# Performance work log

Hardware: AMD Instinct MI355X
Metric: run time of the kernel (lower is better)

Reference implementation:

```python
import jax, jax.numpy as jnp
import numpy as np

# SymBranch: delta_i = |h_i - h_pi(i)| (0 if unpaired) -> ResNetMLP -> per-graph
# mean pairwise-L2 scores -> softmax(s/tau) -> weighted sum pooling.
# ResNetMLP (reconstructed, eval mode: dropout=identity):
#   h = x @ W_in + b_in
#   for each block: h = h + relu(LN(h @ Wk + bk))
#   z = LN_out(h @ W_out + b_out)   (last_norm=True)

B, NPG, IN_DIM, HID, EMB, NBLK = 64, 1024, 64, 256, 128, 3
TAU = 0.25
LN_EPS = 1e-5


def _ln(x, g, b):
    mu = jnp.mean(x, axis=-1, keepdims=True)
    var = jnp.var(x, axis=-1, keepdims=True)
    return (x - mu) * jax.lax.rsqrt(var + LN_EPS) * g + b


def setup_inputs() -> dict:
    key = jax.random.key(0)
    ks = jax.random.split(key, 8)
    N = B * NPG
    H = jax.random.normal(ks[0], (N, IN_DIM), jnp.float32)
    batch_ptr = jnp.arange(B + 1, dtype=jnp.int32) * NPG  # equal-size graphs
    # symmetric pairs: node i in first half of each graph paired with i + NPG/2
    half = NPG // 2
    base = (jnp.arange(B, dtype=jnp.int32) * NPG)[:, None]
    li = (base + jnp.arange(half, dtype=jnp.int32)[None, :]).reshape(-1)
    ri = (base + half + jnp.arange(half, dtype=jnp.int32)[None, :]).reshape(-1)
    pairs = jnp.stack([li, ri], axis=1)  # [M,2] global indices
    W_in = jax.random.normal(ks[1], (IN_DIM, HID), jnp.float32) * (1.0 / np.sqrt(IN_DIM))
    b_in = jnp.zeros((HID,), jnp.float32)
    Wb = jax.random.normal(ks[2], (NBLK, HID, HID), jnp.float32) * (1.0 / np.sqrt(HID))
    bb = jnp.zeros((NBLK, HID), jnp.float32)
    lng = jnp.ones((NBLK, HID), jnp.float32)
    lnb = jnp.zeros((NBLK, HID), jnp.float32)
    W_out = jax.random.normal(ks[3], (HID, EMB), jnp.float32) * (1.0 / np.sqrt(HID))
    b_out = jnp.zeros((EMB,), jnp.float32)
    lnf_g = jnp.ones((EMB,), jnp.float32)
    lnf_b = jnp.zeros((EMB,), jnp.float32)
    return dict(H=H, batch_ptr=batch_ptr, pairs=pairs, W_in=W_in, b_in=b_in,
                Wb=Wb, bb=bb, lng=lng, lnb=lnb, W_out=W_out, b_out=b_out,
                lnf_g=lnf_g, lnf_b=lnf_b)


def reference(H, batch_ptr, pairs, W_in, b_in, Wb, bb, lng, lnb, W_out, b_out, lnf_g, lnf_b):
    # gather-diff-scatter: delta_i = |h_i - h_pair(i)|, 0 for unpaired nodes
    li, ri = pairs[:, 0], pairs[:, 1]
    diff = jnp.abs(H[li] - H[ri])                       # [M, in_dim]
    delta = jnp.zeros_like(H).at[li].set(diff).at[ri].set(diff)  # [N, in_dim]
    # ResNetMLP (eval: dropout off)
    h = delta @ W_in + b_in                             # [N, HID]
    for k in range(NBLK):
        h = h + jax.nn.relu(_ln(h @ Wb[k] + bb[k], lng[k], lnb[k]))
    z = _ln(h @ W_out + b_out, lnf_g, lnf_b)            # [N, EMB]
    # per-graph mean pairwise L2 (graphs are equal-sized: reshape is the batched
    # equivalent of the python loop over batch_ptr slices)
    zb = z.reshape(B, NPG, EMB)
    sq = jnp.sum(zb * zb, axis=-1)                      # [B, n]
    d2 = sq[:, :, None] + sq[:, None, :] - 2.0 * jnp.einsum('bne,bme->bnm', zb, zb)
    dist = jnp.sqrt(jnp.clip(d2, 1e-12))                # [B, n, n]
    s = jnp.mean(dist, axis=-1)                         # [B, n]
    w = jax.nn.softmax(s / TAU, axis=-1)                # [B, n]
    f = jnp.einsum('bn,bne->be', w, zb)                 # [B, EMB]
    return f, w
```

## Files before the change

### kernel.cpp

```cpp
#include <hip/hip_runtime.h>
#include <hip/hip_bf16.h>

using bf16 = __hip_bfloat16;
typedef __attribute__((ext_vector_type(8))) short  bfrag;
typedef __attribute__((ext_vector_type(4))) float  ffrag;

#define DEVFN static __device__ __forceinline__

constexpr int BATCH  = 64;
constexpr int NPG    = 1024;
constexpr int IN_DIM = 64;
constexpr int HID    = 256;
constexpr int EMB    = 128;
constexpr int NPAIR  = BATCH * NPG / 2;
constexpr float TAU    = 0.25f;
constexpr float LN_EPS = 1e-5f;

constexpr int LDH = 264;

DEVFN float b2f(unsigned short u) {
    union { unsigned int i; float f; } x; x.i = ((unsigned int)u) << 16; return x.f;
}
DEVFN unsigned short f2b(float f) {
    bf16 h = __float2bfloat16(f);
    unsigned short u; __builtin_memcpy(&u, &h, 2); return u;
}

__global__ __launch_bounds__(256) void prep_w_kernel(
    const float* __restrict__ Win, const float* __restrict__ Wb,
    const float* __restrict__ Wout,
    unsigned short* __restrict__ WinT, unsigned short* __restrict__ WbT,
    unsigned short* __restrict__ WoutT)
{
    __shared__ short t[64][72];
    const int bid = blockIdx.x, tid = threadIdx.x;
    const float* S; unsigned short* D; int N_, K_, k0, n0;
    if (bid < 48) {
        int mat = bid >> 4, tt = bid & 15;
        S = Wb + mat * 65536; D = WbT + mat * 65536;
        K_ = 256; N_ = 256; k0 = (tt >> 2) * 64; n0 = (tt & 3) * 64;
    } else if (bid < 52) {
        int tt = bid - 48;
        S = Win; D = WinT; K_ = 64; N_ = 256; k0 = 0; n0 = tt * 64;
    } else {
        int tt = bid - 52;
        S = Wout; D = WoutT; K_ = 256; N_ = 128; k0 = (tt >> 1) * 64; n0 = (tt & 1) * 64;
    }
    #pragma unroll
    for (int it = 0; it < 4; ++it) {
        int idx = it * 256 + tid;
        int kk = idx >> 4, n4 = idx & 15;
        float4 v = *(const float4*)(S + (size_t)(k0 + kk) * N_ + n0 + n4 * 4);
        t[n4 * 4 + 0][kk] = (short)f2b(v.x);
        t[n4 * 4 + 1][kk] = (short)f2b(v.y);
        t[n4 * 4 + 2][kk] = (short)f2b(v.z);
        t[n4 * 4 + 3][kk] = (short)f2b(v.w);
    }
    __syncthreads();
    const int KB = K_ >> 5, nb = n0 >> 6;
    #pragma unroll
    for (int it = 0; it < 2; ++it) {
        int u = it * 256 + tid;
        int kbL = u >> 8, rem = u & 255;
        int j = rem >> 6, ln = rem & 63;
        int l16 = ln & 15, qd = ln >> 4;
        bfrag val = *(const bfrag*)&t[j * 16 + l16][kbL * 32 + qd * 8];
        size_t dst = (((size_t)(nb * KB + (k0 >> 5) + kbL) * 4 + j) * 64 + ln) * 8;
        *(bfrag*)(D + dst) = val;
    }
}

template<int K, int N, int MODE>
DEVFN void gemm_phase(short* hbuf, float (*part)[8],
                      const unsigned short* __restrict__ Bf,
                      const float* __restrict__ bias,
                      const float* __restrict__ gamma,
                      const float* __restrict__ beta,
                      unsigned short* __restrict__ Zb,
                      float* __restrict__ sqout, int m0)
{
    constexpr int WN = N / 64;
    constexpr int WM = 4 / WN;
    constexpr int RM = (64 / WM) / 16;
    constexpr int RN = 4;
    constexpr int KB = K / 32;

    const int tid  = threadIdx.x;
    const int wave = tid >> 6, lane = tid & 63;
    const int quad = lane >> 4, l16 = lane & 15;
    const int wrow = (wave / WN) * (64 / WM);
    const int wcol = (wave % WN) * 64;

    __syncthreads();

    ffrag acc[RM][RN];
    #pragma unroll
    for (int i = 0; i < RM; i++)
        #pragma unroll
        for (int j = 0; j < RN; j++)
            #pragma unroll
            for (int r = 0; r < 4; r++) acc[i][j][r] = 0.f;

    const unsigned short* bq = Bf + (size_t)(wcol >> 6) * KB * 2048
                                  + (size_t)lane * 8;

    bfrag acur[RM], bcur[RN];
    #pragma unroll
    for (int j = 0; j < RN; j++)
        bcur[j] = *(const bfrag*)(bq + j * 512);
    #pragma unroll
    for (int i = 0; i < RM; i++)
        acur[i] = *(const bfrag*)&hbuf[(wrow + i * 16 + l16) * LDH + quad * 8];

    #pragma unroll
    for (int kb = 0; kb < KB; kb++) {
        bfrag anx[RM], bnx[RN];
        if (kb + 1 < KB) {
            #pragma unroll
            for (int j = 0; j < RN; j++)
                bnx[j] = *(const bfrag*)(bq + ((kb + 1) * 4 + j) * 512);
            #pragma unroll
            for (int i = 0; i < RM; i++)
                anx[i] = *(const bfrag*)&hbuf[(wrow + i * 16 + l16) * LDH
                                              + (kb + 1) * 32 + quad * 8];
        }
        #pragma unroll
        for (int i = 0; i < RM; i++)
            #pragma unroll
            for (int j = 0; j < RN; j++)
                acc[i][j] = __builtin_amdgcn_mfma_f32_16x16x32_bf16(
                                acur[i], bcur[j], acc[i][j], 0, 0, 0);
        if (kb + 1 < KB) {
            #pragma unroll
            for (int i = 0; i < RM; i++) acur[i] = anx[i];
            #pragma unroll
            for (int j = 0; j < RN; j++) bcur[j] = bnx[j];
        }
    }

    float bia[RN], gam[RN], bet[RN];
    #pragma unroll
    for (int j = 0; j < RN; j++) {
        int gcol = wcol + j * 16 + l16;
        bia[j] = bias[gcol];
        if constexpr (MODE != 0) { gam[j] = gamma[gcol]; bet[j] = beta[gcol]; }
    }
    #pragma unroll
    for (int i = 0; i < RM; i++)
        #pragma unroll
        for (int j = 0; j < RN; j++)
            #pragma unroll
            for (int r = 0; r < 4; r++) acc[i][j][r] += bia[j];

    if constexpr (MODE == 0) {
        __syncthreads();
        #pragma unroll
        for (int i = 0; i < RM; i++)
            #pragma unroll
            for (int j = 0; j < RN; j++) {
                int gcol = wcol + j * 16 + l16;
                #pragma unroll
                for (int r = 0; r < 4; r++) {
                    int row = wrow + i * 16 + quad * 4 + r;
                    hbuf[row * LDH + gcol] = (short)f2b(acc[i][j][r]);
                }
            }
    } else {
        #pragma unroll
        for (int i = 0; i < RM; i++) {
            #pragma unroll
            for (int r = 0; r < 4; r++) {
                float s1 = 0.f, s2 = 0.f;
                #pragma unroll
                for (int j = 0; j < RN; j++) {
                    float x = acc[i][j][r]; s1 += x; s2 += x * x;
                }
                #pragma unroll
                for (int m = 1; m < 16; m <<= 1) {
                    s1 += __shfl_xor(s1, m); s2 += __shfl_xor(s2, m);
                }
                if (l16 == 0) {
                    int row = wrow + i * 16 + quad * 4 + r;
                    part[row][(wave % WN) * 2]     = s1;
                    part[row][(wave % WN) * 2 + 1] = s2;
                }
            }
        }
        __syncthreads();
        float s3a[RM][4];
        #pragma unroll
        for (int i = 0; i < RM; i++) {
            #pragma unroll
            for (int r = 0; r < 4; r++) {
                int row = wrow + i * 16 + quad * 4 + r;
                float s1 = 0.f, s2 = 0.f;
                #pragma unroll
                for (int wn = 0; wn < WN; wn++) {
                    s1 += part[row][wn * 2]; s2 += part[row][wn * 2 + 1];
                }
                float mean = s1 * (1.f / N);
                float rstd = rsqrtf(s2 * (1.f / N) - mean * mean + LN_EPS);
                float s3 = 0.f;
                #pragma unroll
                for (int j = 0; j < RN; j++) {
                    int gcol = wcol + j * 16 + l16;
                    float y = (acc[i][j][r] - mean) * rstd * gam[j] + bet[j];
                    if constexpr (MODE == 1) {
                        float res = b2f((unsigned short)hbuf[row * LDH + gcol]);
                        y = fmaxf(y, 0.f) + res;
                        hbuf[row * LDH + gcol] = (short)f2b(y);
                    } else {
                        unsigned short ub = f2b(y);
                        Zb[(size_t)(m0 + row) * EMB + gcol] = ub;
                        float yr = b2f(ub);
                        s3 += yr * yr;
                    }
                }
                s3a[i][r] = s3;
            }
        }
        if constexpr (MODE == 2) {
            __syncthreads();
            #pragma unroll
            for (int i = 0; i < RM; i++)
                #pragma unroll
                for (int r = 0; r < 4; r++) {
                    float s3 = s3a[i][r];
                    #pragma unroll
                    for (int m = 1; m < 16; m <<= 1) s3 += __shfl_xor(s3, m);
                    if (l16 == 0) {
                        int row = wrow + i * 16 + quad * 4 + r;
                        part[row][wave % WN] = s3;
                    }
                }
            __syncthreads();
            if (l16 == 0 && (wave % WN) == 0) {
                #pragma unroll
                for (int i = 0; i < RM; i++)
                    #pragma unroll
                    for (int r = 0; r < 4; r++) {
                        int row = wrow + i * 16 + quad * 4 + r;
                        float t = 0.f;
                        #pragma unroll
                        for (int wn = 0; wn < WN; wn++) t += part[row][wn];
                        sqout[m0 + row] = t;
                    }
            }
        }
    }
}

__global__ __launch_bounds__(256, 3) void fused_mlp_kernel(
    const float* __restrict__ H, const int* __restrict__ pairs,
    const unsigned short* __restrict__ WinT,
    const unsigned short* __restrict__ WbT,
    const unsigned short* __restrict__ WoutT,
    const float* __restrict__ b_in,  const float* __restrict__ bb,
    const float* __restrict__ lng,   const float* __restrict__ lnb,
    const float* __restrict__ b_out, const float* __restrict__ lnf_g,
    const float* __restrict__ lnf_b,
    unsigned short* __restrict__ Zb, float* __restrict__ sq)
{
    __shared__ __align__(16) short hbuf[64 * LDH];
    __shared__ float part[64][8];

    const int tid = threadIdx.x;
    const int m0  = blockIdx.x * 64;

    #pragma unroll
    for (int it = 0; it < 4; ++it) {
        int idx = tid + it * 256;
        int r = idx >> 4, c4 = idx & 15;
        int p = m0 + r;
        int li = pairs[2 * p], ri = pairs[2 * p + 1];
        float4 a = *(const float4*)(H + (size_t)li * IN_DIM + c4 * 4);
        float4 b = *(const float4*)(H + (size_t)ri * IN_DIM + c4 * 4);
        short4 s;
        s.x = (short)f2b(fabsf(a.x - b.x));
        s.y = (short)f2b(fabsf(a.y - b.y));
        s.z = (short)f2b(fabsf(a.z - b.z));
        s.w = (short)f2b(fabsf(a.w - b.w));
        *(short4*)&hbuf[r * LDH + c4 * 4] = s;
    }

    gemm_phase<IN_DIM, HID, 0>(hbuf, part, WinT, b_in,
                               nullptr, nullptr, nullptr, nullptr, m0);
    gemm_phase<HID, HID, 1>(hbuf, part, WbT,
                            bb,       lng,       lnb,       nullptr, nullptr, m0);
    gemm_phase<HID, HID, 1>(hbuf, part, WbT + 65536,
                            bb + 256, lng + 256, lnb + 256, nullptr, nullptr, m0);
    gemm_phase<HID, HID, 1>(hbuf, part, WbT + 131072,
                            bb + 512, lng + 512, lnb + 512, nullptr, nullptr, m0);
    gemm_phase<HID, EMB, 2>(hbuf, part, WoutT, b_out,
                            lnf_g, lnf_b, Zb, sq, m0);
}

__global__ __launch_bounds__(256) void gram_kernel(
    const unsigned short* __restrict__ Z, const float* __restrict__ sq,
    float* __restrict__ srowP)
{
    constexpr int LDU = EMB + 8;
    __shared__ __align__(16) short Brows[64 * LDU];

    const int batch = blockIdx.x >> 4;
    const int rt    = (blockIdx.x >> 1) & 7;
    const int hf    = blockIdx.x & 1;
    const int tid = threadIdx.x, wave = tid >> 6, lane = tid & 63;
    const int quad = lane >> 4, l16 = lane & 15;
    const int urow0 = batch * 512;
    const int ar0   = urow0 + rt * 64;
    const int arow  = ar0 + wave * 16 + l16;

    bfrag a4[4];
    #pragma unroll
    for (int kk = 0; kk < 4; kk++)
        a4[kk] = *(const bfrag*)(Z + (size_t)arow * EMB + kk * 32 + quad * 8);

    float rs[4] = {0.f, 0.f, 0.f, 0.f};
    float sqr[4];
    #pragma unroll
    for (int r = 0; r < 4; r++)
        sqr[r] = sq[ar0 + wave * 16 + quad * 4 + r];

    for (int c = 0; c < 4; ++c) {
        int ch = hf * 4 + c;
        __syncthreads();
        #pragma unroll
        for (int it = 0; it < 4; ++it) {
            int idx = tid + it * 256;
            int r = idx >> 4, cc = (idx & 15) * 8;
            *(bfrag*)&Brows[r * LDU + cc] =
                *(const bfrag*)(Z + (size_t)(urow0 + ch * 64 + r) * EMB + cc);
        }
        __syncthreads();
        ffrag acc[4];
        #pragma unroll
        for (int j = 0; j < 4; j++)
            #pragma unroll
            for (int r = 0; r < 4; r++) acc[j][r] = 0.f;
        #pragma unroll
        for (int kk = 0; kk < 4; ++kk)
            #pragma unroll
            for (int j = 0; j < 4; j++) {
                bfrag b = *(const bfrag*)&Brows[(j * 16 + l16) * LDU
                                                + kk * 32 + quad * 8];
                acc[j] = __builtin_amdgcn_mfma_f32_16x16x32_bf16(a4[kk], b,
                                                                 acc[j], 0, 0, 0);
            }
        #pragma unroll
        for (int j = 0; j < 4; j++) {
            float sqc = sq[urow0 + ch * 64 + j * 16 + l16];
            #pragma unroll
            for (int r = 0; r < 4; r++) {
                float d2 = sqr[r] + sqc - 2.f * acc[j][r];
                rs[r] += sqrtf(fmaxf(d2, 1e-12f));
            }
        }
    }
    #pragma unroll
    for (int r = 0; r < 4; r++) {
        float v = rs[r];
        v += __shfl_xor(v, 1); v += __shfl_xor(v, 2);
        v += __shfl_xor(v, 4); v += __shfl_xor(v, 8);
        if (l16 == 0)
            srowP[hf * (BATCH * 512) + batch * 512 + rt * 64
                  + wave * 16 + quad * 4 + r] = v;
    }
}

__global__ __launch_bounds__(1024) void softmax_f_kernel(
    const float* __restrict__ srowP, const unsigned short* __restrict__ Z,
    float* __restrict__ fout, float* __restrict__ wout)
{
    const int b = blockIdx.x, tid = threadIdx.x;
    __shared__ float wsh[512];
    __shared__ float red[16];
    __shared__ float fred[8][128];
    constexpr float SC = (1.f / 512.f) * (1.f / TAU);

    const int wv = tid >> 6, lane = tid & 63;
    float l0 = 0.f, e0 = 0.f;
    if (tid < 512) {
        l0 = (srowP[b * 512 + tid] + srowP[BATCH * 512 + b * 512 + tid]) * SC;
        float mx = l0;
        #pragma unroll
        for (int m = 1; m < 64; m <<= 1) mx = fmaxf(mx, __shfl_xor(mx, m));
        if (lane == 0) red[wv] = mx;
    }
    __syncthreads();
    float mx = red[0];
    #pragma unroll
    for (int i = 1; i < 8; i++) mx = fmaxf(mx, red[i]);
    if (tid < 512) {
        e0 = expf(l0 - mx);
        float s = e0;
        #pragma unroll
        for (int m = 1; m < 64; m <<= 1) s += __shfl_xor(s, m);
        if (lane == 0) red[8 + wv] = s;
    }
    __syncthreads();
    float sum = 0.f;
    #pragma unroll
    for (int i = 0; i < 8; i++) sum += red[8 + i];
    float inv = 1.f / sum;
    if (tid < 512) wsh[tid] = e0 * inv;
    __syncthreads();
    wout[b * 1024 + tid] = wsh[tid & 511] * 0.5f;

    const int g = tid >> 7, e = tid & 127;
    const unsigned short* zp = Z + (size_t)(b * 512 + g * 64) * EMB + e;
    float acc = 0.f;
    #pragma unroll 8
    for (int c = 0; c < 64; c++)
        acc += wsh[g * 64 + c] * b2f(zp[(size_t)c * EMB]);
    fred[g][e] = acc;
    __syncthreads();
    if (tid < 128) {
        float t = 0.f;
        #pragma unroll
        for (int gg = 0; gg < 8; gg++) t += fred[gg][e];
        fout[b * EMB + e] = t;
    }
}

extern "C" void kernel_launch(void* const* d_in, const int* in_sizes, int n_in,
                              void* d_out, int out_size, void* d_ws, size_t ws_size,
                              hipStream_t stream)
{
    (void)in_sizes; (void)n_in; (void)out_size; (void)ws_size;
    const float* H     = (const float*)d_in[0];
    const int*   pairs = (const int*)d_in[2];
    const float* W_in  = (const float*)d_in[3];
    const float* b_in  = (const float*)d_in[4];
    const float* Wb    = (const float*)d_in[5];
    const float* bb    = (const float*)d_in[6];
    const float* lng   = (const float*)d_in[7];
    const float* lnb   = (const float*)d_in[8];
    const float* W_out = (const float*)d_in[9];
    const float* b_out = (const float*)d_in[10];
    const float* lnf_g = (const float*)d_in[11];
    const float* lnf_b = (const float*)d_in[12];

    float* f_out = (float*)d_out;
    float* w_out = (float*)d_out + BATCH * EMB;

    char* ws = (char*)d_ws;
    size_t off = 0;
    auto carve = [&](size_t bytes) -> void* {
        void* p = ws + off;
        off += (bytes + 255) & ~(size_t)255;
        return p;
    };
    unsigned short* WinT  = (unsigned short*)carve((size_t)HID * IN_DIM * 2);
    unsigned short* WbT   = (unsigned short*)carve((size_t)3 * HID * HID * 2);
    unsigned short* WoutT = (unsigned short*)carve((size_t)EMB * HID * 2);
    unsigned short* Zb    = (unsigned short*)carve((size_t)NPAIR * EMB * 2);
    float*          sq    = (float*)carve((size_t)NPAIR * 4);
    float*          srowP = (float*)carve((size_t)2 * BATCH * 512 * 4);

    prep_w_kernel<<<60, 256, 0, stream>>>(W_in, Wb, W_out, WinT, WbT, WoutT);

    fused_mlp_kernel<<<NPAIR / 64, 256, 0, stream>>>(
        H, pairs, WinT, WbT, WoutT,
        b_in, bb, lng, lnb, b_out, lnf_g, lnf_b, Zb, sq);

    gram_kernel<<<BATCH * 16, 256, 0, stream>>>(Zb, sq, srowP);
    softmax_f_kernel<<<BATCH, 1024, 0, stream>>>(srowP, Zb, f_out, w_out);
}
```

Baseline: 150.4 us.

## Halve MLP row tile, deepen weight prefetch, double-buffer gram kernel B tiles

```diff
diff --git a/kernel.cpp b/kernel.cpp
--- a/kernel.cpp
+++ b/kernel.cpp
@@ -16,6 +16,7 @@
 constexpr float TAU    = 0.25f;
 constexpr float LN_EPS = 1e-5f;
 
+constexpr int MT  = 32;
 constexpr int LDH = 264;
 
 DEVFN float b2f(unsigned short u) {
@@ -81,14 +82,14 @@
 {
     constexpr int WN = N / 64;
     constexpr int WM = 4 / WN;
-    constexpr int RM = (64 / WM) / 16;
+    constexpr int RM = (MT / WM) / 16;
     constexpr int RN = 4;
     constexpr int KB = K / 32;
 
     const int tid  = threadIdx.x;
     const int wave = tid >> 6, lane = tid & 63;
     const int quad = lane >> 4, l16 = lane & 15;
-    const int wrow = (wave / WN) * (64 / WM);
+    const int wrow = (wave / WN) * (MT / WM);
     const int wcol = (wave % WN) * 64;
 
     __syncthreads();
@@ -104,21 +105,28 @@
     const unsigned short* bq = Bf + (size_t)(wcol >> 6) * KB * 2048
                                   + (size_t)lane * 8;
 
-    bfrag acur[RM], bcur[RN];
+    bfrag b0[RN], b1[RN], b2[RN];
+    bfrag acur[RM], anx[RM];
     #pragma unroll
     for (int j = 0; j < RN; j++)
-        bcur[j] = *(const bfrag*)(bq + j * 512);
+        b0[j] = *(const bfrag*)(bq + j * 512);
+    if constexpr (KB > 1) {
+        #pragma unroll
+        for (int j = 0; j < RN; j++)
+            b1[j] = *(const bfrag*)(bq + (4 + j) * 512);
+    }
     #pragma unroll
     for (int i = 0; i < RM; i++)
         acur[i] = *(const bfrag*)&hbuf[(wrow + i * 16 + l16) * LDH + quad * 8];
 
     #pragma unroll
     for (int kb = 0; kb < KB; kb++) {
-        bfrag anx[RM], bnx[RN];
+        if (kb + 2 < KB) {
+            #pragma unroll
+            for (int j = 0; j < RN; j++)
+                b2[j] = *(const bfrag*)(bq + ((kb + 2) * 4 + j) * 512);
+        }
         if (kb + 1 < KB) {
-            #pragma unroll
-            for (int j = 0; j < RN; j++)
-                bnx[j] = *(const bfrag*)(bq + ((kb + 1) * 4 + j) * 512);
             #pragma unroll
             for (int i = 0; i < RM; i++)
                 anx[i] = *(const bfrag*)&hbuf[(wrow + i * 16 + l16) * LDH
@@ -129,12 +137,12 @@
             #pragma unroll
             for (int j = 0; j < RN; j++)
                 acc[i][j] = __builtin_amdgcn_mfma_f32_16x16x32_bf16(
-                                acur[i], bcur[j], acc[i][j], 0, 0, 0);
+                                acur[i], b0[j], acc[i][j], 0, 0, 0);
         if (kb + 1 < KB) {
             #pragma unroll
+            for (int j = 0; j < RN; j++) { b0[j] = b1[j]; b1[j] = b2[j]; }
+            #pragma unroll
             for (int i = 0; i < RM; i++) acur[i] = anx[i];
-            #pragma unroll
-            for (int j = 0; j < RN; j++) bcur[j] = bnx[j];
         }
     }
 
@@ -261,14 +269,14 @@
     const float* __restrict__ lnf_b,
     unsigned short* __restrict__ Zb, float* __restrict__ sq)
 {
-    __shared__ __align__(16) short hbuf[64 * LDH];
-    __shared__ float part[64][8];
+    __shared__ __align__(16) short hbuf[MT * LDH];
+    __shared__ float part[MT][8];
 
     const int tid = threadIdx.x;
-    const int m0  = blockIdx.x * 64;
-
-    #pragma unroll
-    for (int it = 0; it < 4; ++it) {
+    const int m0  = blockIdx.x * MT;
+
+    #pragma unroll
+    for (int it = 0; it < 2; ++it) {
         int idx = tid + it * 256;
         int r = idx >> 4, c4 = idx & 15;
         int p = m0 + r;
@@ -300,7 +308,7 @@
     float* __restrict__ srowP)
 {
     constexpr int LDU = EMB + 8;
-    __shared__ __align__(16) short Brows[64 * LDU];
+    __shared__ __align__(16) short Brows[2][64 * LDU];
 
     const int batch = blockIdx.x >> 4;
     const int rt    = (blockIdx.x >> 1) & 7;
@@ -322,17 +330,25 @@
     for (int r = 0; r < 4; r++)
         sqr[r] = sq[ar0 + wave * 16 + quad * 4 + r];
 
+    const int sr = tid >> 4, sc = (tid & 15) * 8;
+    bfrag g[4];
+    #pragma unroll
+    for (int it = 0; it < 4; ++it)
+        g[it] = *(const bfrag*)(Z + (size_t)(urow0 + hf * 256 + it * 16 + sr) * EMB + sc);
+
     for (int c = 0; c < 4; ++c) {
+        const int cur = c & 1;
+        #pragma unroll
+        for (int it = 0; it < 4; ++it)
+            *(bfrag*)&Brows[cur][(it * 16 + sr) * LDU + sc] = g[it];
+        if (c < 3) {
+            #pragma unroll
+            for (int it = 0; it < 4; ++it)
+                g[it] = *(const bfrag*)(Z + (size_t)(urow0 + hf * 256 + (c + 1) * 64
+                                                     + it * 16 + sr) * EMB + sc);
+        }
+        __syncthreads();
         int ch = hf * 4 + c;
-        __syncthreads();
-        #pragma unroll
-        for (int it = 0; it < 4; ++it) {
-            int idx = tid + it * 256;
-            int r = idx >> 4, cc = (idx & 15) * 8;
-            *(bfrag*)&Brows[r * LDU + cc] =
-                *(const bfrag*)(Z + (size_t)(urow0 + ch * 64 + r) * EMB + cc);
-        }
-        __syncthreads();
         ffrag acc[4];
         #pragma unroll
         for (int j = 0; j < 4; j++)
@@ -342,8 +358,8 @@
         for (int kk = 0; kk < 4; ++kk)
             #pragma unroll
             for (int j = 0; j < 4; j++) {
-                bfrag b = *(const bfrag*)&Brows[(j * 16 + l16) * LDU
-                                                + kk * 32 + quad * 8];
+                bfrag b = *(const bfrag*)&Brows[cur][(j * 16 + l16) * LDU
+                                                     + kk * 32 + quad * 8];
                 acc[j] = __builtin_amdgcn_mfma_f32_16x16x32_bf16(a4[kk], b,
                                                                  acc[j], 0, 0, 0);
             }
@@ -460,7 +476,7 @@
 
     prep_w_kernel<<<60, 256, 0, stream>>>(W_in, Wb, W_out, WinT, WbT, WoutT);
 
-    fused_mlp_kernel<<<NPAIR / 64, 256, 0, stream>>>(
+    fused_mlp_kernel<<<NPAIR / MT, 256, 0, stream>>>(
         H, pairs, WinT, WbT, WoutT,
         b_in, bb, lng, lnb, b_out, lnf_g, lnf_b, Zb, sq);
 
```

After: 142.5 us. 1.06x faster.
